# Performance work log

Measured on AMD Instinct MI355X. Metric: run time of the kernel, lower is better.

The kernel has to match this reference:

```python
import jax, jax.numpy as jnp
import numpy as np

N_HEADS = 8

def setup_inputs() -> dict:
    key = jax.random.key(0)
    qkv = jax.random.normal(key, (4, 1536, 2048), dtype=jnp.float32)
    return {"qkv": qkv}

def reference(qkv):
    bs, width, length = qkv.shape
    ch = width // (3 * N_HEADS)
    q, k, v = jnp.split(qkv, 3, axis=1)  # each [bs, H*C, T]
    scale = 1.0 / np.sqrt(ch).astype(np.float32)
    q = (q * scale).reshape(bs * N_HEADS, ch, length)
    k = k.reshape(bs * N_HEADS, ch, length)
    v = v.reshape(bs * N_HEADS, ch, length)
    weight = jnp.einsum('bct,bcs->bts', q, k)  # [bs*H, T, T]
    weight = jax.nn.softmax(weight.astype(jnp.float32), axis=-1).astype(weight.dtype)
    a = jnp.einsum('bts,bcs->bct', weight, v)  # [bs*H, C, T]
    return a.reshape(bs, -1, length)
```

## Files before the change

### kernel.cpp

```cpp
#include <hip/hip_runtime.h>
#include <hip/hip_bf16.h>

typedef unsigned short u16;
typedef unsigned int uint;
typedef __bf16 bf16x8 __attribute__((ext_vector_type(8)));
typedef float f32x16 __attribute__((ext_vector_type(16)));

#define SEQ 2048
#define DH  64

__device__ __forceinline__ u16 f2bf(float x) {
  __bf16 h = (__bf16)x;
  return __builtin_bit_cast(u16, h);
}

#define FSW(r) ((((r) & 3) << 1) | (((r) >> 2) & 1))

__global__ __launch_bounds__(256) void prepass(const float* __restrict__ qkv,
                                               u16* __restrict__ kT,
                                               u16* __restrict__ vB) {
  int idx = blockIdx.x;
  __shared__ float tile[64][65];
  if (idx < 1024) {
    int bh = idx >> 5;
    int t0 = (idx & 31) * 64;
    int b = bh >> 3, h = bh & 7;
    const float* src = qkv + ((size_t)(b*1536 + 512 + h*64)) * SEQ;
    u16* dst = kT + (size_t)bh * SEQ * DH;

    int tl = threadIdx.x & 63;
    int cw = threadIdx.x >> 6;
#pragma unroll
    for (int i = 0; i < 16; ++i) {
      int c = cw + 4*i;
      tile[c][tl] = src[(size_t)c*SEQ + t0 + tl];
    }
    __syncthreads();
    int cl2 = (threadIdx.x & 31) * 2;
    int tw  = threadIdx.x >> 5;
#pragma unroll
    for (int i = 0; i < 8; ++i) {
      int t = tw + 8*i;
      unsigned int lo = f2bf(tile[cl2][t]);
      unsigned int hi = f2bf(tile[cl2+1][t]);
      *(unsigned int*)(dst + (size_t)(t0 + t)*DH + cl2) = lo | (hi << 16);
    }
  } else {
    int row = idx - 1024;
    int bh = row >> 6, c = row & 63;
    int b = bh >> 3, h = bh & 7;
    const float4* src = (const float4*)(qkv + ((size_t)(b*1536 + 1024 + h*64 + c)) * SEQ);
    u16* dst = vB + (size_t)row * SEQ;
    int tid = threadIdx.x;
    float4 a = src[tid*2];
    float4 bq = src[tid*2+1];
    union { u16 u[8]; int4 v4; } pk;
    pk.u[0]=f2bf(a.x); pk.u[1]=f2bf(a.y); pk.u[2]=f2bf(a.z); pk.u[3]=f2bf(a.w);
    pk.u[4]=f2bf(bq.x); pk.u[5]=f2bf(bq.y); pk.u[6]=f2bf(bq.z); pk.u[7]=f2bf(bq.w);
    *(int4*)(dst + tid*8) = pk.v4;
  }
}

__global__ __launch_bounds__(256, 4) void attn(const float* __restrict__ qkv,
                                               const u16* __restrict__ kT,
                                               const u16* __restrict__ vB,
                                               float* __restrict__ out) {
  const int lb = (blockIdx.x & 7) * 128 + (blockIdx.x >> 3);
  const int bh = lb >> 5;
  const int t0 = (lb & 31) * 64;
  const int tid  = threadIdx.x;
  const int wave = tid >> 6;
  const int th   = wave & 1;
  const int sh   = wave >> 1;
  const int lane = tid & 63;
  const int l31  = lane & 31;
  const int hi   = lane >> 5;

  __shared__ __align__(16) u16 smem[2][2][64*64];

  bf16x8 bq[4];
  {
    float* qtile = (float*)&smem[0][0][0];
    const float* qsrc = qkv + ((size_t)((bh >> 3)*1536 + (bh & 7)*64)) * SEQ + t0;
    const float qscale = 0.1803368801111244f;
    int qc = tid >> 2, tb = (tid & 3) * 16;
    const float4* s4 = (const float4*)(qsrc + (size_t)qc*SEQ + tb);
    float4 v0 = s4[0], v1 = s4[1], v2 = s4[2], v3 = s4[3];
    float* qd = qtile + qc*65 + tb;
    qd[0]=v0.x*qscale; qd[1]=v0.y*qscale; qd[2]=v0.z*qscale; qd[3]=v0.w*qscale;
    qd[4]=v1.x*qscale; qd[5]=v1.y*qscale; qd[6]=v1.z*qscale; qd[7]=v1.w*qscale;
    qd[8]=v2.x*qscale; qd[9]=v2.y*qscale; qd[10]=v2.z*qscale; qd[11]=v2.w*qscale;
    qd[12]=v3.x*qscale; qd[13]=v3.y*qscale; qd[14]=v3.z*qscale; qd[15]=v3.w*qscale;
    __syncthreads();
    int tloc = th*32 + l31;
#pragma unroll
    for (int kb = 0; kb < 4; ++kb) {
      uint dd[4];
#pragma unroll
      for (int e = 0; e < 4; ++e) {
        float lo = qtile[(kb*16 + hi*8 + 2*e    )*65 + tloc];
        float hh = qtile[(kb*16 + hi*8 + 2*e + 1)*65 + tloc];
        asm("v_cvt_pk_bf16_f32 %0, %1, %2" : "=v"(dd[e]) : "v"(lo), "v"(hh));
      }
      uint4 u = {dd[0], dd[1], dd[2], dd[3]};
      bq[kb] = __builtin_bit_cast(bf16x8, u);
    }
    __syncthreads();
  }

  const uint4 uones = {0x3F803F80u, 0x3F803F80u, 0x3F803F80u, 0x3F803F80u};
  const bf16x8 aone = __builtin_bit_cast(bf16x8, uones);
  const f32x16 fzero = {};

  const u16* ksrc0 = kT + (size_t)bh*SEQ*DH;
  const u16* vsrc0 = vB + (size_t)bh*DH*SEQ;
  const int ci0 = (wave*2+0)*64 + lane;
  const int ci1 = (wave*2+1)*64 + lane;
  const int kr0 = ci0 >> 3, kc0 = ci0 & 7;
  const int kr1 = ci1 >> 3, kc1 = ci1 & 7;
  const u16* kg0 = ksrc0 + (size_t)kr0*DH + ((kc0 ^ FSW(kr0)) * 8);
  const u16* kg1 = ksrc0 + (size_t)kr1*DH + ((kc1 ^ FSW(kr1)) * 8);
  const u16* vg0 = vsrc0 + (size_t)kr0*SEQ + ((kc0 ^ FSW(kr0)) * 8);
  const u16* vg1 = vsrc0 + (size_t)kr1*SEQ + ((kc1 ^ FSW(kr1)) * 8);

#define GLDS(src, dst) __builtin_amdgcn_global_load_lds(                        \
    (const __attribute__((address_space(1))) unsigned int*)(src),               \
    (__attribute__((address_space(3))) unsigned int*)(dst), 16, 0, 0)
#define STAGE(b, sbase) do {                                                    \
    GLDS(kg0 + (size_t)(sbase)*DH, &smem[b][0][ci0*8]);                         \
    GLDS(kg1 + (size_t)(sbase)*DH, &smem[b][0][ci1*8]);                         \
    GLDS(vg0 + (sbase),            &smem[b][1][ci0*8]);                         \
    GLDS(vg1 + (sbase),            &smem[b][1][ci1*8]);                         \
  } while (0)

  const int fl = FSW(l31);
  const u16* kP0 = &smem[0][0][(sh*32 + l31)*64 + (((0+hi) ^ fl) * 8)];
  const u16* kP1 = &smem[0][0][(sh*32 + l31)*64 + (((2+hi) ^ fl) * 8)];
  const u16* kP2 = &smem[0][0][(sh*32 + l31)*64 + (((4+hi) ^ fl) * 8)];
  const u16* kP3 = &smem[0][0][(sh*32 + l31)*64 + (((6+hi) ^ fl) * 8)];
  const u16* vP00 = &smem[0][1][l31*64      + (((sh*4 + 0 + hi) ^ fl) * 8)];
  const u16* vP01 = &smem[0][1][l31*64      + (((sh*4 + 2 + hi) ^ fl) * 8)];
  const u16* vP10 = &smem[0][1][(32+l31)*64 + (((sh*4 + 0 + hi) ^ fl) * 8)];
  const u16* vP11 = &smem[0][1][(32+l31)*64 + (((sh*4 + 2 + hi) ^ fl) * 8)];

  f32x16 acc0 = {}, acc1 = {}, lacc = {};

  STAGE(0, 0);
  __syncthreads();

#define TILEBODY(B, DO_STAGE, SNEXT) do {                                       \
    if (DO_STAGE) STAGE(B ^ 1, SNEXT);                                          \
    f32x16 S0 = __builtin_amdgcn_mfma_f32_32x32x16_bf16(                        \
        *(const bf16x8*)(kP0 + (B)*8192), bq[0], fzero, 0, 0, 0);               \
    __builtin_amdgcn_s_setprio(1);                                              \
    S0 = __builtin_amdgcn_mfma_f32_32x32x16_bf16(                               \
        *(const bf16x8*)(kP1 + (B)*8192), bq[1], S0, 0, 0, 0);                  \
    S0 = __builtin_amdgcn_mfma_f32_32x32x16_bf16(                               \
        *(const bf16x8*)(kP2 + (B)*8192), bq[2], S0, 0, 0, 0);                  \
    S0 = __builtin_amdgcn_mfma_f32_32x32x16_bf16(                               \
        *(const bf16x8*)(kP3 + (B)*8192), bq[3], S0, 0, 0, 0);                  \
    __builtin_amdgcn_s_setprio(0);                                              \
    float p0[16];                                                               \
    _Pragma("unroll")                                                           \
    for (int i = 0; i < 16; ++i) p0[i] = __builtin_amdgcn_exp2f(S0[i]);         \
    uint d0[8];                                                                 \
    _Pragma("unroll")                                                           \
    for (int q = 0; q < 4; ++q) {                                               \
      asm("v_cvt_pk_bf16_f32 %0, %1, %2" : "=v"(d0[2*q+0]) : "v"(p0[4*q+0]), "v"(p0[4*q+1])); \
      asm("v_cvt_pk_bf16_f32 %0, %1, %2" : "=v"(d0[2*q+1]) : "v"(p0[4*q+2]), "v"(p0[4*q+3])); \
    }                                                                           \
    bf16x8 pf0, pf1;                                                            \
    {                                                                           \
      uint X0 = d0[0], X1 = d0[1], Y0 = d0[2], Y1 = d0[3];                      \
      asm("v_permlane32_swap_b32 %0, %1" : "+v"(X0), "+v"(Y0));                 \
      asm("v_permlane32_swap_b32 %0, %1" : "+v"(X1), "+v"(Y1));                 \
      uint4 u = {X0, X1, Y0, Y1};                                               \
      pf0 = __builtin_bit_cast(bf16x8, u);                                      \
    }                                                                           \
    {                                                                           \
      uint X0 = d0[4], X1 = d0[5], Y0 = d0[6], Y1 = d0[7];                      \
      asm("v_permlane32_swap_b32 %0, %1" : "+v"(X0), "+v"(Y0));                 \
      asm("v_permlane32_swap_b32 %0, %1" : "+v"(X1), "+v"(Y1));                 \
      uint4 u = {X0, X1, Y0, Y1};                                               \
      pf1 = __builtin_bit_cast(bf16x8, u);                                      \
    }                                                                           \
    __builtin_amdgcn_s_setprio(1);                                              \
    acc0 = __builtin_amdgcn_mfma_f32_32x32x16_bf16(                             \
        *(const bf16x8*)(vP00 + (B)*8192), pf0, acc0, 0, 0, 0);                 \
    acc1 = __builtin_amdgcn_mfma_f32_32x32x16_bf16(                             \
        *(const bf16x8*)(vP10 + (B)*8192), pf0, acc1, 0, 0, 0);                 \
    lacc = __builtin_amdgcn_mfma_f32_32x32x16_bf16(aone, pf0, lacc, 0, 0, 0);   \
    acc0 = __builtin_amdgcn_mfma_f32_32x32x16_bf16(                             \
        *(const bf16x8*)(vP01 + (B)*8192), pf1, acc0, 0, 0, 0);                 \
    acc1 = __builtin_amdgcn_mfma_f32_32x32x16_bf16(                             \
        *(const bf16x8*)(vP11 + (B)*8192), pf1, acc1, 0, 0, 0);                 \
    lacc = __builtin_amdgcn_mfma_f32_32x32x16_bf16(aone, pf1, lacc, 0, 0, 0);   \
    __builtin_amdgcn_s_setprio(0);                                              \
    __syncthreads();                                                            \
  } while (0)

  for (int s0 = 0; s0 < SEQ; s0 += 128) {
    TILEBODY(0, true, s0 + 64);
    TILEBODY(1, s0 + 128 < SEQ, s0 + 128);
  }
#undef TILEBODY
#undef STAGE
#undef GLDS

  float* ep = (float*)&smem[0][0][0];
  float* lp = ep + 4*1024;
  if (sh == 1) {
    float* b0 = ep + (th*2+0)*1024 + lane;
    float* b1 = ep + (th*2+1)*1024 + lane;
#pragma unroll
    for (int r = 0; r < 16; ++r) { b0[r*64] = acc0[r]; b1[r*64] = acc1[r]; }
    lp[th*64 + lane] = lacc[0];
  }
  __syncthreads();
  if (sh == 0) {
    const float* b0 = ep + (th*2+0)*1024 + lane;
    const float* b1 = ep + (th*2+1)*1024 + lane;
#pragma unroll
    for (int r = 0; r < 16; ++r) { acc0[r] += b0[r*64]; acc1[r] += b1[r*64]; }
    float lt = lacc[0] + lp[th*64 + lane];
    float linv = 1.0f / lt;
    float* ob = out + (size_t)(bh*64) * SEQ + t0 + th*32 + l31;
#pragma unroll
    for (int r = 0; r < 16; ++r) {
      int c0 = (r & 3) + 8*(r >> 2) + 4*hi;
      ob[(size_t)c0 * SEQ]        = acc0[r] * linv;
      ob[(size_t)(32 + c0) * SEQ] = acc1[r] * linv;
    }
  }
}

extern "C" void kernel_launch(void* const* d_in, const int* in_sizes, int n_in,
                              void* d_out, int out_size, void* d_ws, size_t ws_size,
                              hipStream_t stream) {
  const float* qkv = (const float*)d_in[0];
  float* out = (float*)d_out;
  u16* kT = (u16*)d_ws;
  u16* vB = kT + (size_t)32*SEQ*DH;
  prepass<<<3072, 256, 0, stream>>>(qkv, kT, vB);
  attn<<<1024, 256, 0, stream>>>(qkv, kT, vB, out);
}
```

Baseline: 61.90 us.

## Fuse V bf16 conversion into attention kernel, drop V prepass

Removes the V-conversion half of the prepass. The attention kernel now loads fp32 V directly from qkv into registers, converts it to bf16 and writes it to the swizzled LDS buffer after the PV MFMAs, which gives software prefetch overlap. This removes a global write and re-read of the bf16 V copy, plus 2048 prepass blocks. In exchange, every attention block (32 per head) rereads its head's fp32 V, doubling that traffic, and it adds register pressure and VALU conversion work inside the main loop.

```diff
diff --git a/kernel.cpp b/kernel.cpp
--- a/kernel.cpp
+++ b/kernel.cpp
@@ -17,53 +17,36 @@
 #define FSW(r) ((((r) & 3) << 1) | (((r) >> 2) & 1))
 
 __global__ __launch_bounds__(256) void prepass(const float* __restrict__ qkv,
-                                               u16* __restrict__ kT,
-                                               u16* __restrict__ vB) {
+                                               u16* __restrict__ kT) {
   int idx = blockIdx.x;
   __shared__ float tile[64][65];
-  if (idx < 1024) {
-    int bh = idx >> 5;
-    int t0 = (idx & 31) * 64;
-    int b = bh >> 3, h = bh & 7;
-    const float* src = qkv + ((size_t)(b*1536 + 512 + h*64)) * SEQ;
-    u16* dst = kT + (size_t)bh * SEQ * DH;
-
-    int tl = threadIdx.x & 63;
-    int cw = threadIdx.x >> 6;
-#pragma unroll
-    for (int i = 0; i < 16; ++i) {
-      int c = cw + 4*i;
-      tile[c][tl] = src[(size_t)c*SEQ + t0 + tl];
-    }
-    __syncthreads();
-    int cl2 = (threadIdx.x & 31) * 2;
-    int tw  = threadIdx.x >> 5;
-#pragma unroll
-    for (int i = 0; i < 8; ++i) {
-      int t = tw + 8*i;
-      unsigned int lo = f2bf(tile[cl2][t]);
-      unsigned int hi = f2bf(tile[cl2+1][t]);
-      *(unsigned int*)(dst + (size_t)(t0 + t)*DH + cl2) = lo | (hi << 16);
-    }
-  } else {
-    int row = idx - 1024;
-    int bh = row >> 6, c = row & 63;
-    int b = bh >> 3, h = bh & 7;
-    const float4* src = (const float4*)(qkv + ((size_t)(b*1536 + 1024 + h*64 + c)) * SEQ);
-    u16* dst = vB + (size_t)row * SEQ;
-    int tid = threadIdx.x;
-    float4 a = src[tid*2];
-    float4 bq = src[tid*2+1];
-    union { u16 u[8]; int4 v4; } pk;
-    pk.u[0]=f2bf(a.x); pk.u[1]=f2bf(a.y); pk.u[2]=f2bf(a.z); pk.u[3]=f2bf(a.w);
-    pk.u[4]=f2bf(bq.x); pk.u[5]=f2bf(bq.y); pk.u[6]=f2bf(bq.z); pk.u[7]=f2bf(bq.w);
-    *(int4*)(dst + tid*8) = pk.v4;
+  int bh = idx >> 5;
+  int t0 = (idx & 31) * 64;
+  int b = bh >> 3, h = bh & 7;
+  const float* src = qkv + ((size_t)(b*1536 + 512 + h*64)) * SEQ;
+  u16* dst = kT + (size_t)bh * SEQ * DH;
+
+  int tl = threadIdx.x & 63;
+  int cw = threadIdx.x >> 6;
+#pragma unroll
+  for (int i = 0; i < 16; ++i) {
+    int c = cw + 4*i;
+    tile[c][tl] = src[(size_t)c*SEQ + t0 + tl];
+  }
+  __syncthreads();
+  int cl2 = (threadIdx.x & 31) * 2;
+  int tw  = threadIdx.x >> 5;
+#pragma unroll
+  for (int i = 0; i < 8; ++i) {
+    int t = tw + 8*i;
+    unsigned int lo = f2bf(tile[cl2][t]);
+    unsigned int hi = f2bf(tile[cl2+1][t]);
+    *(unsigned int*)(dst + (size_t)(t0 + t)*DH + cl2) = lo | (hi << 16);
   }
 }
 
 __global__ __launch_bounds__(256, 4) void attn(const float* __restrict__ qkv,
                                                const u16* __restrict__ kT,
-                                               const u16* __restrict__ vB,
                                                float* __restrict__ out) {
   const int lb = (blockIdx.x & 7) * 128 + (blockIdx.x >> 3);
   const int bh = lb >> 5;
@@ -113,24 +96,37 @@
   const f32x16 fzero = {};
 
   const u16* ksrc0 = kT + (size_t)bh*SEQ*DH;
-  const u16* vsrc0 = vB + (size_t)bh*DH*SEQ;
+  const float* vsrc0 = qkv + ((size_t)((bh >> 3)*1536 + 1024 + (bh & 7)*64)) * SEQ;
   const int ci0 = (wave*2+0)*64 + lane;
   const int ci1 = (wave*2+1)*64 + lane;
   const int kr0 = ci0 >> 3, kc0 = ci0 & 7;
   const int kr1 = ci1 >> 3, kc1 = ci1 & 7;
   const u16* kg0 = ksrc0 + (size_t)kr0*DH + ((kc0 ^ FSW(kr0)) * 8);
   const u16* kg1 = ksrc0 + (size_t)kr1*DH + ((kc1 ^ FSW(kr1)) * 8);
-  const u16* vg0 = vsrc0 + (size_t)kr0*SEQ + ((kc0 ^ FSW(kr0)) * 8);
-  const u16* vg1 = vsrc0 + (size_t)kr1*SEQ + ((kc1 ^ FSW(kr1)) * 8);
+  const float* vq0 = vsrc0 + (size_t)kr0*SEQ + ((kc0 ^ FSW(kr0)) * 8);
+  const float* vq1 = vsrc0 + (size_t)kr1*SEQ + ((kc1 ^ FSW(kr1)) * 8);
 
 #define GLDS(src, dst) __builtin_amdgcn_global_load_lds(                        \
     (const __attribute__((address_space(1))) unsigned int*)(src),               \
     (__attribute__((address_space(3))) unsigned int*)(dst), 16, 0, 0)
-#define STAGE(b, sbase) do {                                                    \
+#define STAGEK(b, sbase) do {                                                   \
     GLDS(kg0 + (size_t)(sbase)*DH, &smem[b][0][ci0*8]);                         \
     GLDS(kg1 + (size_t)(sbase)*DH, &smem[b][0][ci1*8]);                         \
-    GLDS(vg0 + (sbase),            &smem[b][1][ci0*8]);                         \
-    GLDS(vg1 + (sbase),            &smem[b][1][ci1*8]);                         \
+  } while (0)
+#define VSTORE(b) do {                                                          \
+    uint e0,e1,e2,e3,e4,e5,e6,e7;                                               \
+    asm("v_cvt_pk_bf16_f32 %0, %1, %2" : "=v"(e0) : "v"(w0.x), "v"(w0.y));      \
+    asm("v_cvt_pk_bf16_f32 %0, %1, %2" : "=v"(e1) : "v"(w0.z), "v"(w0.w));      \
+    asm("v_cvt_pk_bf16_f32 %0, %1, %2" : "=v"(e2) : "v"(w1.x), "v"(w1.y));      \
+    asm("v_cvt_pk_bf16_f32 %0, %1, %2" : "=v"(e3) : "v"(w1.z), "v"(w1.w));      \
+    asm("v_cvt_pk_bf16_f32 %0, %1, %2" : "=v"(e4) : "v"(w2.x), "v"(w2.y));      \
+    asm("v_cvt_pk_bf16_f32 %0, %1, %2" : "=v"(e5) : "v"(w2.z), "v"(w2.w));      \
+    asm("v_cvt_pk_bf16_f32 %0, %1, %2" : "=v"(e6) : "v"(w3.x), "v"(w3.y));      \
+    asm("v_cvt_pk_bf16_f32 %0, %1, %2" : "=v"(e7) : "v"(w3.z), "v"(w3.w));      \
+    uint4 u0 = {e0, e1, e2, e3};                                                \
+    uint4 u1 = {e4, e5, e6, e7};                                                \
+    *(uint4*)(&smem[b][1][ci0*8]) = u0;                                         \
+    *(uint4*)(&smem[b][1][ci1*8]) = u1;                                         \
   } while (0)
 
   const int fl = FSW(l31);
@@ -145,11 +141,25 @@
 
   f32x16 acc0 = {}, acc1 = {}, lacc = {};
 
-  STAGE(0, 0);
+  {
+    STAGEK(0, 0);
+    float4 w0 = *(const float4*)(vq0);
+    float4 w1 = *(const float4*)(vq0 + 4);
+    float4 w2 = *(const float4*)(vq1);
+    float4 w3 = *(const float4*)(vq1 + 4);
+    VSTORE(0);
+  }
   __syncthreads();
 
 #define TILEBODY(B, DO_STAGE, SNEXT) do {                                       \
-    if (DO_STAGE) STAGE(B ^ 1, SNEXT);                                          \
+    float4 w0, w1, w2, w3;                                                      \
+    if (DO_STAGE) {                                                             \
+      STAGEK(B ^ 1, SNEXT);                                                     \
+      w0 = *(const float4*)(vq0 + (SNEXT));                                     \
+      w1 = *(const float4*)(vq0 + (SNEXT) + 4);                                 \
+      w2 = *(const float4*)(vq1 + (SNEXT));                                     \
+      w3 = *(const float4*)(vq1 + (SNEXT) + 4);                                 \
+    }                                                                           \
     f32x16 S0 = __builtin_amdgcn_mfma_f32_32x32x16_bf16(                        \
         *(const bf16x8*)(kP0 + (B)*8192), bq[0], fzero, 0, 0, 0);               \
     __builtin_amdgcn_s_setprio(1);                                              \
@@ -196,6 +206,7 @@
         *(const bf16x8*)(vP11 + (B)*8192), pf1, acc1, 0, 0, 0);                 \
     lacc = __builtin_amdgcn_mfma_f32_32x32x16_bf16(aone, pf1, lacc, 0, 0, 0);   \
     __builtin_amdgcn_s_setprio(0);                                              \
+    if (DO_STAGE) VSTORE(B ^ 1);                                                \
     __syncthreads();                                                            \
   } while (0)
 
@@ -204,7 +215,8 @@
     TILEBODY(1, s0 + 128 < SEQ, s0 + 128);
   }
 #undef TILEBODY
-#undef STAGE
+#undef STAGEK
+#undef VSTORE
 #undef GLDS
 
   float* ep = (float*)&smem[0][0][0];
@@ -240,7 +252,6 @@
   const float* qkv = (const float*)d_in[0];
   float* out = (float*)d_out;
   u16* kT = (u16*)d_ws;
-  u16* vB = kT + (size_t)32*SEQ*DH;
-  prepass<<<3072, 256, 0, stream>>>(qkv, kT, vB);
-  attn<<<1024, 256, 0, stream>>>(qkv, kT, vB, out);
-}
+  prepass<<<1024, 256, 0, stream>>>(qkv, kT);
+  attn<<<1024, 256, 0, stream>>>(qkv, kT, out);
+}
```

New measurement: 102.6 us. 65.7% more time.
